# Optimization experiments

Hardware: AMD Instinct MI355X
Metric: run time of the kernel (lower is better)

## Reference

```python
import jax, jax.numpy as jnp
import numpy as np

B, S, E, H, L, NH, OUT = 32, 512, 512, 512, 2, 8, 1
HD = E // NH  # head dim


def setup_inputs() -> dict:
    key = jax.random.key(0)
    ks = jax.random.split(key, 16)
    sc_e = 1.0 / np.sqrt(E)
    sc_h = 1.0 / np.sqrt(H)
    inp = {
        "x": jax.random.normal(ks[0], (B, S, E), dtype=jnp.float32),
        "Wq": jax.random.normal(ks[1], (E, E), dtype=jnp.float32) * sc_e,
        "bq": jnp.zeros((E,), dtype=jnp.float32),
        "Wk": jax.random.normal(ks[2], (E, E), dtype=jnp.float32) * sc_e,
        "bk": jnp.zeros((E,), dtype=jnp.float32),
        "Wv": jax.random.normal(ks[3], (E, E), dtype=jnp.float32) * sc_e,
        "bv": jnp.zeros((E,), dtype=jnp.float32),
        "Wo": jax.random.normal(ks[4], (E, E), dtype=jnp.float32) * sc_e,
        "bo": jnp.zeros((E,), dtype=jnp.float32),
        # stacked RNN cell params (layer 0 input = E = H, so all layers share shape)
        "Wih": jax.random.normal(ks[5], (L, H, H), dtype=jnp.float32) * sc_h,
        "bih": jnp.zeros((L, H), dtype=jnp.float32),
        "Whh": jax.random.normal(ks[6], (L, H, H), dtype=jnp.float32) * sc_h,
        "bhh": jnp.zeros((L, H), dtype=jnp.float32),
        "Wfc": jax.random.normal(ks[7], (OUT, H), dtype=jnp.float32) * sc_h,
        "bfc": jnp.zeros((OUT,), dtype=jnp.float32),
    }
    return inp


def _forward(x, Wq, bq, Wk, bk, Wv, bv, Wo, bo, Wih, bih, Whh, bhh, Wfc, bfc):
    # Multi-head attention (self-attention, no mask; dropout = identity in eval)
    Q = (x @ Wq.T + bq).reshape(B, S, NH, HD)
    K = (x @ Wk.T + bk).reshape(B, S, NH, HD)
    V = (x @ Wv.T + bv).reshape(B, S, NH, HD)
    scores = jnp.einsum("bqhd,bkhd->bhqk", Q, K) / jnp.sqrt(jnp.float32(HD))
    attn = jax.nn.softmax(scores, axis=-1)
    ctx = jnp.einsum("bhqk,bkhd->bqhd", attn, V).reshape(B, S, E)
    atten_out = ctx @ Wo.T + bo  # [B, S, E]

    # Multi-layer Elman RNN scan over time; only last-step hidden is used.
    h0 = jnp.zeros((L, B, H), dtype=x.dtype)

    def step(h, x_t):
        inp = x_t
        new_h = []
        for i in range(L):
            inp = jnp.tanh(inp @ Wih[i].T + bih[i] + h[i] @ Whh[i].T + bhh[i])
            new_h.append(inp)
        return jnp.stack(new_h), None

    h_final, _ = jax.lax.scan(step, h0, jnp.swapaxes(atten_out, 0, 1))  # scan over S
    return h_final[-1] @ Wfc.T + bfc  # [B, OUT]


def reference(x, Wq, bq, Wk, bk, Wv, bv, Wo, bo, Wih, bih, Whh, bhh, Wfc, bfc):
    return _forward(x, Wq, bq, Wk, bk, Wv, bv, Wo, bo, Wih, bih, Whh, bhh, Wfc, bfc)
```

## Files before the change

kernel.cpp:

```cpp
#include <hip/hip_runtime.h>
#include <hip/hip_fp16.h>

#define B 32
#define S 512
#define E 512
#define H 512
#define NH 8
#define HD 64
#define POISON 0x7FC0DEADu

typedef _Float16 h16x8 __attribute__((ext_vector_type(8)));
typedef _Float16 h16x4 __attribute__((ext_vector_type(4)));
typedef _Float16 h16x2 __attribute__((ext_vector_type(2)));
typedef float f32x4 __attribute__((ext_vector_type(4)));

#if __has_builtin(__builtin_amdgcn_fdot2)
__device__ __forceinline__ float dot2f(h16x2 a, h16x2 b, float c) {
    return __builtin_amdgcn_fdot2(a, b, c, false);
}
#else
__device__ __forceinline__ float dot2f(h16x2 a, h16x2 b, float c) {
    return c + (float)a[0] * (float)b[0] + (float)a[1] * (float)b[1];
}
#endif

__device__ __forceinline__ h16x2 pr(h16x8 v, int q) {
    h16x2 r; r[0] = v[2 * q]; r[1] = v[2 * q + 1]; return r;
}

__global__ __launch_bounds__(256) void cast_h(const float* __restrict__ src,
                                              _Float16* __restrict__ dst, int n4) {
    int i = blockIdx.x * 256 + threadIdx.x;
    const int stride = gridDim.x * 256;
    for (; i < n4; i += stride) {
        float4 v = ((const float4*)src)[i];
        h16x4 o;
        o[0] = (_Float16)v.x; o[1] = (_Float16)v.y;
        o[2] = (_Float16)v.z; o[3] = (_Float16)v.w;
        ((h16x4*)dst)[i] = o;
    }
}

template <int OMODE>
__global__ __launch_bounds__(256) void gemm_mfma(const _Float16* __restrict__ A,
                                                 const _Float16* __restrict__ W,
                                                 const float* __restrict__ bias,
                                                 void* __restrict__ Cout,
                                                 int M, int N, int K) {
    __shared__ __align__(16) _Float16 Als[128 * 32];
    __shared__ __align__(16) _Float16 Bls[128 * 32];
    const int tid = threadIdx.x;
    const int m0 = blockIdx.y * 128;
    const int n0 = blockIdx.x * 128;
    const int lane = tid & 63;
    const int w = tid >> 6;
    const int wm = w >> 1, wn = w & 1;
    f32x4 acc[4][4] = {};

    const int srow = tid >> 1;
    const int shalf = tid & 1;
    const _Float16* Ag = A + (size_t)(m0 + srow) * K + shalf * 16;
    const _Float16* Wg = W + (size_t)(n0 + srow) * K + shalf * 16;

    for (int k0 = 0; k0 < K; k0 += 32) {
        h16x8 a0 = *(const h16x8*)(Ag + k0);
        h16x8 a1 = *(const h16x8*)(Ag + k0 + 8);
        h16x8 b0 = *(const h16x8*)(Wg + k0);
        h16x8 b1 = *(const h16x8*)(Wg + k0 + 8);
        __syncthreads();
        *(h16x8*)&Als[srow * 32 + shalf * 16] = a0;
        *(h16x8*)&Als[srow * 32 + shalf * 16 + 8] = a1;
        *(h16x8*)&Bls[srow * 32 + shalf * 16] = b0;
        *(h16x8*)&Bls[srow * 32 + shalf * 16 + 8] = b1;
        __syncthreads();
        h16x8 af[4], bf[4];
#pragma unroll
        for (int mt = 0; mt < 4; ++mt)
            af[mt] = *(const h16x8*)&Als[(wm * 64 + mt * 16 + (lane & 15)) * 32 + (lane >> 4) * 8];
#pragma unroll
        for (int nt = 0; nt < 4; ++nt)
            bf[nt] = *(const h16x8*)&Bls[(wn * 64 + nt * 16 + (lane & 15)) * 32 + (lane >> 4) * 8];
#pragma unroll
        for (int mt = 0; mt < 4; ++mt)
#pragma unroll
            for (int nt = 0; nt < 4; ++nt)
                acc[mt][nt] = __builtin_amdgcn_mfma_f32_16x16x32_f16(af[mt], bf[nt], acc[mt][nt], 0, 0, 0);
    }

    float* Cf = (float*)Cout;
    _Float16* Ch = (_Float16*)Cout;
    const int colb = n0 + wn * 64 + (lane & 15);
    const int rowb = m0 + wm * 64 + ((lane >> 4) << 2);
#pragma unroll
    for (int mt = 0; mt < 4; ++mt) {
#pragma unroll
        for (int nt = 0; nt < 4; ++nt) {
            const int c = colb + nt * 16;
            const float bv = bias[c];
            if (OMODE == 2) {
                const int R0 = rowb + mt * 16;
                const int bb = R0 >> 9, s = R0 & 511, hh = c >> 6, d = c & 63;
                h16x4 pk;
#pragma unroll
                for (int j = 0; j < 4; ++j) pk[j] = (_Float16)(acc[mt][nt][j] + bv);
                *(h16x4*)&Ch[((size_t)(bb * 8 + hh) * 64 + d) * 512 + s] = pk;
            } else {
#pragma unroll
                for (int j = 0; j < 4; ++j) {
                    const int R = rowb + mt * 16 + j;
                    const float v = acc[mt][nt][j] + bv;
                    if (OMODE == 0) Cf[(size_t)R * N + c] = v;
                    else if (OMODE == 3) Cf[((size_t)(R & 511) * 32 + (R >> 9)) * N + c] = v;
                    else Ch[(size_t)R * N + c] = (_Float16)v;
                }
            }
        }
    }
}

__global__ __launch_bounds__(256) void attn_mfma(_Float16* __restrict__ Qb,
                                                 const _Float16* __restrict__ Kb,
                                                 const _Float16* __restrict__ Vt) {
    __shared__ __align__(16) _Float16 Qs[64 * 72];
    __shared__ __align__(16) _Float16 Ks[64 * 72];
    __shared__ __align__(16) _Float16 Vs[64 * 72];
    __shared__ __align__(16) _Float16 Ps[4 * 16 * 72];
    const int tid = threadIdx.x;
    const int lane = tid & 63;
    const int w = tid >> 6;
    const int qt = blockIdx.x & 7;
    const int h = (blockIdx.x >> 3) & 7;
    const int b = blockIdx.x >> 6;
    const size_t qrow0 = (size_t)b * 512 + qt * 64;
    const int col0 = h * 64;

    {
        const int r = tid >> 2;
        const int c0 = (tid & 3) << 4;
        const _Float16* gq = &Qb[(qrow0 + r) * 512 + col0 + c0];
        *(h16x8*)&Qs[r * 72 + c0] = *(const h16x8*)(gq);
        *(h16x8*)&Qs[r * 72 + c0 + 8] = *(const h16x8*)(gq + 8);
    }
    __syncthreads();
    h16x8 aq[2];
#pragma unroll
    for (int ks = 0; ks < 2; ++ks)
        aq[ks] = *(const h16x8*)&Qs[(w * 16 + (lane & 15)) * 72 + ks * 32 + (lane >> 4) * 8];

    float m[4] = {-1e30f, -1e30f, -1e30f, -1e30f};
    float l[4] = {0.f, 0.f, 0.f, 0.f};
    f32x4 acco[4] = {};

    for (int kt = 0; kt < 8; ++kt) {
        __syncthreads();
        {
            const int r = tid >> 2;
            const int c0 = (tid & 3) << 4;
            const _Float16* gk = &Kb[((size_t)b * 512 + kt * 64 + r) * 512 + col0 + c0];
            *(h16x8*)&Ks[r * 72 + c0] = *(const h16x8*)(gk);
            *(h16x8*)&Ks[r * 72 + c0 + 8] = *(const h16x8*)(gk + 8);
            const _Float16* gv = &Vt[((size_t)(b * 8 + h) * 64 + r) * 512 + kt * 64 + c0];
            *(h16x8*)&Vs[r * 72 + c0] = *(const h16x8*)(gv);
            *(h16x8*)&Vs[r * 72 + c0 + 8] = *(const h16x8*)(gv + 8);
        }
        __syncthreads();
        f32x4 accs[4] = {};
#pragma unroll
        for (int nt = 0; nt < 4; ++nt) {
#pragma unroll
            for (int ks = 0; ks < 2; ++ks) {
                h16x8 bk = *(const h16x8*)&Ks[(nt * 16 + (lane & 15)) * 72 + ks * 32 + (lane >> 4) * 8];
                accs[nt] = __builtin_amdgcn_mfma_f32_16x16x32_f16(aq[ks], bk, accs[nt], 0, 0, 0);
            }
        }
#pragma unroll
        for (int j = 0; j < 4; ++j) {
            float v = fmaxf(fmaxf(accs[0][j], accs[1][j]), fmaxf(accs[2][j], accs[3][j]));
#pragma unroll
            for (int o = 1; o < 16; o <<= 1) v = fmaxf(v, __shfl_xor(v, o, 64));
            const float mn = fmaxf(m[j], v);
            const float scl = __expf(0.125f * (m[j] - mn));
            m[j] = mn;
            l[j] *= scl;
#pragma unroll
            for (int nt2 = 0; nt2 < 4; ++nt2) acco[nt2][j] *= scl;
            float ps = 0.f;
            const int prow = ((lane >> 4) << 2) + j;
#pragma unroll
            for (int nt = 0; nt < 4; ++nt) {
                const float p = __expf(0.125f * (accs[nt][j] - mn));
                ps += p;
                Ps[w * 16 * 72 + prow * 72 + nt * 16 + (lane & 15)] = (_Float16)p;
            }
#pragma unroll
            for (int o = 1; o < 16; o <<= 1) ps += __shfl_xor(ps, o, 64);
            l[j] += ps;
        }
        __syncthreads();
#pragma unroll
        for (int ks2 = 0; ks2 < 2; ++ks2) {
            h16x8 pa = *(const h16x8*)&Ps[w * 16 * 72 + (lane & 15) * 72 + ks2 * 32 + (lane >> 4) * 8];
#pragma unroll
            for (int nt2 = 0; nt2 < 4; ++nt2) {
                h16x8 bv = *(const h16x8*)&Vs[(nt2 * 16 + (lane & 15)) * 72 + ks2 * 32 + (lane >> 4) * 8];
                acco[nt2] = __builtin_amdgcn_mfma_f32_16x16x32_f16(pa, bv, acco[nt2], 0, 0, 0);
            }
        }
    }
#pragma unroll
    for (int j = 0; j < 4; ++j) {
        const float inv = 1.0f / l[j];
        const size_t r = qrow0 + w * 16 + ((lane >> 4) << 2) + j;
#pragma unroll
        for (int nt2 = 0; nt2 < 4; ++nt2)
            Qb[r * 512 + col0 + nt2 * 16 + (lane & 15)] = (_Float16)(acco[nt2][j] * inv);
    }
}

__global__ __launch_bounds__(256) void fill_poison(uint4* __restrict__ p, int n) {
    const uint4 v = {POISON, POISON, POISON, POISON};
    int i = blockIdx.x * 256 + threadIdx.x;
    const int st = gridDim.x * 256;
    for (; i < n; i += st) p[i] = v;
}

__device__ __forceinline__ unsigned long long poll2(const unsigned* p) {
    unsigned long long v = __hip_atomic_load((const unsigned long long*)p,
                                             __ATOMIC_RELAXED, __HIP_MEMORY_SCOPE_AGENT);
    while ((unsigned)v == POISON || (unsigned)(v >> 32) == POISON) {
        __builtin_amdgcn_s_sleep(1);
        v = __hip_atomic_load((const unsigned long long*)p,
                              __ATOMIC_RELAXED, __HIP_MEMORY_SCOPE_AGENT);
    }
    return v;
}

__global__ __launch_bounds__(256) void rnn_persist(const float* __restrict__ pre,
                                                   const _Float16* __restrict__ W16,
                                                   const float* __restrict__ bhh,
                                                   unsigned* __restrict__ hbuf,
                                                   _Float16* __restrict__ hbuf_h) {
    __shared__ float hl[512];
    __shared__ float part[64][17];
    const int tid = threadIdx.x;
    const int b = blockIdx.x & 31;
    const int sl = blockIdx.x >> 5;
    const int jq = tid & 15, kg = tid >> 4;
    const int jbase = sl * 64, k0 = kg * 32;
    const int j64 = tid & 63;

    const _Float16* w0p = W16 + (size_t)(jbase + jq * 4 + 0) * 512 + k0;
    const _Float16* w1p = W16 + (size_t)(jbase + jq * 4 + 1) * 512 + k0;
    const _Float16* w2p = W16 + (size_t)(jbase + jq * 4 + 2) * 512 + k0;
    const _Float16* w3p = W16 + (size_t)(jbase + jq * 4 + 3) * 512 + k0;
    const float bj = bhh[jbase + j64];

    for (int t = 0; t < S; ++t) {
        h16x8 w0[4], w1[4], w2[4], w3[4];
#pragma unroll
        for (int c8 = 0; c8 < 4; ++c8) {
            w0[c8] = *(const h16x8*)(w0p + c8 * 8);
            w1[c8] = *(const h16x8*)(w1p + c8 * 8);
            w2[c8] = *(const h16x8*)(w2p + c8 * 8);
            w3[c8] = *(const h16x8*)(w3p + c8 * 8);
        }
        const float pv = pre[((size_t)t * 32 + b) * 512 + jbase + j64];
        float a0 = 0.f, a1 = 0.f, a2 = 0.f, a3 = 0.f;
        if (t > 0) {
            const unsigned long long v = poll2(hbuf + (size_t)(t - 1) * (B * H) + b * H + tid * 2);
            hl[tid * 2] = __uint_as_float((unsigned)v);
            hl[tid * 2 + 1] = __uint_as_float((unsigned)(v >> 32));
            __syncthreads();
            f32x4 hw[8];
#pragma unroll
            for (int c = 0; c < 8; ++c) hw[c] = *(const f32x4*)&hl[k0 + c * 4];
            h16x2 hp[16];
#pragma unroll
            for (int c = 0; c < 8; ++c) {
                h16x2 p0, p1;
                p0[0] = (_Float16)hw[c][0]; p0[1] = (_Float16)hw[c][1];
                p1[0] = (_Float16)hw[c][2]; p1[1] = (_Float16)hw[c][3];
                hp[2 * c] = p0; hp[2 * c + 1] = p1;
            }
#pragma unroll
            for (int c8 = 0; c8 < 4; ++c8) {
#pragma unroll
                for (int q = 0; q < 4; ++q) {
                    a0 = dot2f(pr(w0[c8], q), hp[c8 * 4 + q], a0);
                    a1 = dot2f(pr(w1[c8], q), hp[c8 * 4 + q], a1);
                    a2 = dot2f(pr(w2[c8], q), hp[c8 * 4 + q], a2);
                    a3 = dot2f(pr(w3[c8], q), hp[c8 * 4 + q], a3);
                }
            }
        }
        part[jq * 4 + 0][kg] = a0;
        part[jq * 4 + 1][kg] = a1;
        part[jq * 4 + 2][kg] = a2;
        part[jq * 4 + 3][kg] = a3;
        __syncthreads();
        if (tid < 64) {
            float s2 = 0.f;
#pragma unroll
            for (int i = 0; i < 16; ++i) s2 += part[tid][i];
            s2 += bj + pv;
            s2 = fminf(fmaxf(s2, -15.f), 15.f);
            const float ex = __expf(2.f * s2);
            const float hval = (ex - 1.f) / (ex + 1.f);
            const size_t idx = (size_t)t * (B * H) + b * H + jbase + tid;
            __hip_atomic_store(&hbuf[idx], __float_as_uint(hval),
                               __ATOMIC_RELAXED, __HIP_MEMORY_SCOPE_AGENT);
            hbuf_h[idx] = (_Float16)hval;
        }
        __syncthreads();
    }
}

__global__ __launch_bounds__(64) void fc_out(const unsigned* __restrict__ hbits,
                                             const float* __restrict__ Wfc,
                                             const float* __restrict__ bfc,
                                             float* __restrict__ out) {
    int b = blockIdx.x;
    int t = threadIdx.x;
    float a = 0.f;
    for (int j = t; j < 512; j += 64) a += __uint_as_float(hbits[b * 512 + j]) * Wfc[j];
#pragma unroll
    for (int o = 32; o; o >>= 1) a += __shfl_down(a, o, 64);
    if (t == 0) out[b] = a + bfc[0];
}

extern "C" void kernel_launch(void* const* d_in, const int* in_sizes, int n_in,
                              void* d_out, int out_size, void* d_ws, size_t ws_size,
                              hipStream_t stream) {
    const float* x   = (const float*)d_in[0];
    const float* Wq  = (const float*)d_in[1];
    const float* bq  = (const float*)d_in[2];
    const float* Wk  = (const float*)d_in[3];
    const float* bk  = (const float*)d_in[4];
    const float* Wv  = (const float*)d_in[5];
    const float* bv  = (const float*)d_in[6];
    const float* Wo  = (const float*)d_in[7];
    const float* bo  = (const float*)d_in[8];
    const float* Wih = (const float*)d_in[9];
    const float* bih = (const float*)d_in[10];
    const float* Whh = (const float*)d_in[11];
    const float* bhh = (const float*)d_in[12];
    const float* Wfc = (const float*)d_in[13];
    const float* bfc = (const float*)d_in[14];
    float* out = (float*)d_out;
    char* base = (char*)d_ws;

    _Float16* xh   = (_Float16*)(base);
    unsigned* h0u  = (unsigned*)(base);
    _Float16* Qh   = (_Float16*)(base + ((size_t)32 << 20));
    _Float16* h0h  = (_Float16*)(base + ((size_t)32 << 20));
    _Float16* Kh   = (_Float16*)(base + ((size_t)48 << 20));
    unsigned* h1u  = (unsigned*)(base + ((size_t)48 << 20));
    _Float16* Vth  = (_Float16*)(base + ((size_t)64 << 20));
    float*    pre  = (float*)(base + ((size_t)80 << 20));
    _Float16* wgt  = (_Float16*)(base + ((size_t)112 << 20));
    const size_t WSZ = 512 * 512;

    cast_h<<<dim3(4096), dim3(256), 0, stream>>>(x, xh, (B * S * E) / 4);
    cast_h<<<dim3(256), dim3(256), 0, stream>>>(Wq, wgt + 0 * WSZ, WSZ / 4);
    cast_h<<<dim3(256), dim3(256), 0, stream>>>(Wk, wgt + 1 * WSZ, WSZ / 4);
    cast_h<<<dim3(256), dim3(256), 0, stream>>>(Wv, wgt + 2 * WSZ, WSZ / 4);
    cast_h<<<dim3(256), dim3(256), 0, stream>>>(Wo, wgt + 3 * WSZ, WSZ / 4);
    cast_h<<<dim3(256), dim3(256), 0, stream>>>(Wih, wgt + 4 * WSZ, WSZ / 4);
    cast_h<<<dim3(256), dim3(256), 0, stream>>>(Wih + WSZ, wgt + 5 * WSZ, WSZ / 4);
    cast_h<<<dim3(256), dim3(256), 0, stream>>>(Whh, wgt + 6 * WSZ, WSZ / 4);
    cast_h<<<dim3(256), dim3(256), 0, stream>>>(Whh + WSZ, wgt + 7 * WSZ, WSZ / 4);

    const dim3 gg(4, 128), blk(256);
    gemm_mfma<1><<<gg, blk, 0, stream>>>(xh, wgt + 0 * WSZ, bq, Qh, B * S, E, E);
    gemm_mfma<1><<<gg, blk, 0, stream>>>(xh, wgt + 1 * WSZ, bk, Kh, B * S, E, E);
    gemm_mfma<2><<<gg, blk, 0, stream>>>(xh, wgt + 2 * WSZ, bv, Vth, B * S, E, E);
    attn_mfma<<<dim3(B * NH * 8), blk, 0, stream>>>(Qh, Kh, Vth);
    gemm_mfma<1><<<gg, blk, 0, stream>>>(Qh, wgt + 3 * WSZ, bo, Kh, B * S, E, E);
    gemm_mfma<3><<<gg, blk, 0, stream>>>(Kh, wgt + 4 * WSZ, bih, pre, B * S, H, E);

    fill_poison<<<dim3(1024), blk, 0, stream>>>((uint4*)base, (32 << 20) / 16);
    rnn_persist<<<dim3(256), blk, 0, stream>>>(pre, wgt + 6 * WSZ, bhh, h0u, h0h);
    gemm_mfma<0><<<gg, blk, 0, stream>>>(h0h, wgt + 5 * WSZ, bih + 512, pre, B * S, H, H);
    fill_poison<<<dim3(1024), blk, 0, stream>>>((uint4*)(base + ((size_t)48 << 20)),
                                                (32 << 20) / 16);
    rnn_persist<<<dim3(256), blk, 0, stream>>>(pre, wgt + 7 * WSZ, bhh + 512, h1u, h0h);
    fc_out<<<dim3(32), dim3(64), 0, stream>>>(h1u + (size_t)511 * B * H, Wfc, bfc, out);
}
```

Measured before the change: 1.223 ms.

## Fuse both RNN layers into one persistent kernel with LDS-resident recurrent weights

Replaces the two sequential per-layer persistent RNN launches and the intermediate input-projection GEMM with a single 512-block kernel. Half the blocks run layer 0 and half run layer 1, and layer 1 consumes layer 0's hidden states through poll-on-poison as they are produced. Each layer's Whh slice is staged once into swizzled LDS (64KB) instead of being reloaded from global memory every step. Layer 1 now computes its Wih projection inline each step, reading those weights from global memory. The scheme relies on all 512 blocks being co-resident (2 per CU) to avoid deadlock.

```diff
diff --git a/kernel.cpp b/kernel.cpp
--- a/kernel.cpp
+++ b/kernel.cpp
@@ -109,8 +109,7 @@
                 for (int j = 0; j < 4; ++j) {
                     const int R = rowb + mt * 16 + j;
                     const float v = acc[mt][nt][j] + bv;
-                    if (OMODE == 0) Cf[(size_t)R * N + c] = v;
-                    else if (OMODE == 3) Cf[((size_t)(R & 511) * 32 + (R >> 9)) * N + c] = v;
+                    if (OMODE == 3) Cf[((size_t)(R & 511) * 32 + (R >> 9)) * N + c] = v;
                     else Ch[(size_t)R * N + c] = (_Float16)v;
                 }
             }
@@ -235,45 +234,62 @@
     return v;
 }
 
-__global__ __launch_bounds__(256) void rnn_persist(const float* __restrict__ pre,
-                                                   const _Float16* __restrict__ W16,
-                                                   const float* __restrict__ bhh,
-                                                   unsigned* __restrict__ hbuf,
-                                                   _Float16* __restrict__ hbuf_h) {
-    __shared__ float hl[512];
+__global__ __launch_bounds__(256, 2) void rnn_fused2(const float* __restrict__ pre0,
+                                                     const _Float16* __restrict__ Whh0h,
+                                                     const _Float16* __restrict__ Whh1h,
+                                                     const _Float16* __restrict__ Wih1h,
+                                                     const float* __restrict__ bhh,
+                                                     const float* __restrict__ bih,
+                                                     unsigned* __restrict__ h0u,
+                                                     unsigned* __restrict__ h1u) {
+    __shared__ __align__(16) _Float16 Wl[64 * 512];
+    __shared__ float hlA[512];
+    __shared__ float hlB[512];
     __shared__ float part[64][17];
     const int tid = threadIdx.x;
+    const int role = blockIdx.x >> 8;
     const int b = blockIdx.x & 31;
-    const int sl = blockIdx.x >> 5;
+    const int sl = (blockIdx.x >> 5) & 7;
     const int jq = tid & 15, kg = tid >> 4;
     const int jbase = sl * 64, k0 = kg * 32;
     const int j64 = tid & 63;
 
-    const _Float16* w0p = W16 + (size_t)(jbase + jq * 4 + 0) * 512 + k0;
-    const _Float16* w1p = W16 + (size_t)(jbase + jq * 4 + 1) * 512 + k0;
-    const _Float16* w2p = W16 + (size_t)(jbase + jq * 4 + 2) * 512 + k0;
-    const _Float16* w3p = W16 + (size_t)(jbase + jq * 4 + 3) * 512 + k0;
-    const float bj = bhh[jbase + j64];
+    const _Float16* Wsrc = role ? Whh1h : Whh0h;
+#pragma unroll
+    for (int i = 0; i < 16; ++i) {
+        const int e = tid + i * 256;
+        const int row = e >> 6;
+        const int l = e & 63;
+        h16x8 v = *(const h16x8*)&Wsrc[(size_t)(jbase + row) * 512 + l * 8];
+        const int p = (l & 56) | ((l + (row >> 2)) & 7);
+        *(h16x8*)&Wl[row * 512 + p * 8] = v;
+    }
+    const float bconst = role ? (bih[512 + jbase + j64] + bhh[512 + jbase + j64])
+                              : bhh[jbase + j64];
+    unsigned* myH = role ? h1u : h0u;
+    __syncthreads();
 
     for (int t = 0; t < S; ++t) {
-        h16x8 w0[4], w1[4], w2[4], w3[4];
-#pragma unroll
-        for (int c8 = 0; c8 < 4; ++c8) {
-            w0[c8] = *(const h16x8*)(w0p + c8 * 8);
-            w1[c8] = *(const h16x8*)(w1p + c8 * 8);
-            w2[c8] = *(const h16x8*)(w2p + c8 * 8);
-            w3[c8] = *(const h16x8*)(w3p + c8 * 8);
-        }
-        const float pv = pre[((size_t)t * 32 + b) * 512 + jbase + j64];
         float a0 = 0.f, a1 = 0.f, a2 = 0.f, a3 = 0.f;
-        if (t > 0) {
-            const unsigned long long v = poll2(hbuf + (size_t)(t - 1) * (B * H) + b * H + tid * 2);
-            hl[tid * 2] = __uint_as_float((unsigned)v);
-            hl[tid * 2 + 1] = __uint_as_float((unsigned)(v >> 32));
+        float pv = 0.f;
+        if (role == 0) {
+            pv = pre0[((size_t)t * 32 + b) * 512 + jbase + j64];
+        } else {
+            h16x8 ww0[4], ww1[4], ww2[4], ww3[4];
+#pragma unroll
+            for (int c8 = 0; c8 < 4; ++c8) {
+                ww0[c8] = *(const h16x8*)&Wih1h[(size_t)(jbase + jq * 4 + 0) * 512 + k0 + c8 * 8];
+                ww1[c8] = *(const h16x8*)&Wih1h[(size_t)(jbase + jq * 4 + 1) * 512 + k0 + c8 * 8];
+                ww2[c8] = *(const h16x8*)&Wih1h[(size_t)(jbase + jq * 4 + 2) * 512 + k0 + c8 * 8];
+                ww3[c8] = *(const h16x8*)&Wih1h[(size_t)(jbase + jq * 4 + 3) * 512 + k0 + c8 * 8];
+            }
+            const unsigned long long v = poll2(h0u + (size_t)t * (B * H) + b * H + tid * 2);
+            hlA[tid * 2] = __uint_as_float((unsigned)v);
+            hlA[tid * 2 + 1] = __uint_as_float((unsigned)(v >> 32));
             __syncthreads();
             f32x4 hw[8];
 #pragma unroll
-            for (int c = 0; c < 8; ++c) hw[c] = *(const f32x4*)&hl[k0 + c * 4];
+            for (int c = 0; c < 8; ++c) hw[c] = *(const f32x4*)&hlA[k0 + c * 4];
             h16x2 hp[16];
 #pragma unroll
             for (int c = 0; c < 8; ++c) {
@@ -286,11 +302,43 @@
             for (int c8 = 0; c8 < 4; ++c8) {
 #pragma unroll
                 for (int q = 0; q < 4; ++q) {
-                    a0 = dot2f(pr(w0[c8], q), hp[c8 * 4 + q], a0);
-                    a1 = dot2f(pr(w1[c8], q), hp[c8 * 4 + q], a1);
-                    a2 = dot2f(pr(w2[c8], q), hp[c8 * 4 + q], a2);
-                    a3 = dot2f(pr(w3[c8], q), hp[c8 * 4 + q], a3);
+                    a0 = dot2f(pr(ww0[c8], q), hp[c8 * 4 + q], a0);
+                    a1 = dot2f(pr(ww1[c8], q), hp[c8 * 4 + q], a1);
+                    a2 = dot2f(pr(ww2[c8], q), hp[c8 * 4 + q], a2);
+                    a3 = dot2f(pr(ww3[c8], q), hp[c8 * 4 + q], a3);
                 }
+            }
+        }
+        if (t > 0) {
+            const unsigned long long v = poll2(myH + (size_t)(t - 1) * (B * H) + b * H + tid * 2);
+            hlB[tid * 2] = __uint_as_float((unsigned)v);
+            hlB[tid * 2 + 1] = __uint_as_float((unsigned)(v >> 32));
+            __syncthreads();
+            f32x4 hw[8];
+#pragma unroll
+            for (int c = 0; c < 8; ++c) hw[c] = *(const f32x4*)&hlB[k0 + c * 4];
+            h16x2 hp[16];
+#pragma unroll
+            for (int c = 0; c < 8; ++c) {
+                h16x2 p0, p1;
+                p0[0] = (_Float16)hw[c][0]; p0[1] = (_Float16)hw[c][1];
+                p1[0] = (_Float16)hw[c][2]; p1[1] = (_Float16)hw[c][3];
+                hp[2 * c] = p0; hp[2 * c + 1] = p1;
+            }
+#pragma unroll
+            for (int jj = 0; jj < 4; ++jj) {
+                const int r = jq * 4 + jj;
+                float s = 0.f;
+#pragma unroll
+                for (int c8 = 0; c8 < 4; ++c8) {
+                    const int l = kg * 4 + c8;
+                    const int p = (l & 56) | ((l + jq) & 7);
+                    h16x8 w8 = *(const h16x8*)&Wl[r * 512 + p * 8];
+#pragma unroll
+                    for (int q = 0; q < 4; ++q) s = dot2f(pr(w8, q), hp[c8 * 4 + q], s);
+                }
+                if (jj == 0) a0 += s; else if (jj == 1) a1 += s;
+                else if (jj == 2) a2 += s; else a3 += s;
             }
         }
         part[jq * 4 + 0][kg] = a0;
@@ -302,14 +350,13 @@
             float s2 = 0.f;
 #pragma unroll
             for (int i = 0; i < 16; ++i) s2 += part[tid][i];
-            s2 += bj + pv;
+            s2 += bconst + pv;
             s2 = fminf(fmaxf(s2, -15.f), 15.f);
             const float ex = __expf(2.f * s2);
             const float hval = (ex - 1.f) / (ex + 1.f);
-            const size_t idx = (size_t)t * (B * H) + b * H + jbase + tid;
-            __hip_atomic_store(&hbuf[idx], __float_as_uint(hval),
-                               __ATOMIC_RELAXED, __HIP_MEMORY_SCOPE_AGENT);
-            hbuf_h[idx] = (_Float16)hval;
+            __hip_atomic_store(&myH[(size_t)t * (B * H) + b * H + jbase + tid],
+                               __float_as_uint(hval), __ATOMIC_RELAXED,
+                               __HIP_MEMORY_SCOPE_AGENT);
         }
         __syncthreads();
     }
@@ -352,7 +399,6 @@
     _Float16* xh   = (_Float16*)(base);
     unsigned* h0u  = (unsigned*)(base);
     _Float16* Qh   = (_Float16*)(base + ((size_t)32 << 20));
-    _Float16* h0h  = (_Float16*)(base + ((size_t)32 << 20));
     _Float16* Kh   = (_Float16*)(base + ((size_t)48 << 20));
     unsigned* h1u  = (unsigned*)(base + ((size_t)48 << 20));
     _Float16* Vth  = (_Float16*)(base + ((size_t)64 << 20));
@@ -379,10 +425,9 @@
     gemm_mfma<3><<<gg, blk, 0, stream>>>(Kh, wgt + 4 * WSZ, bih, pre, B * S, H, E);
 
     fill_poison<<<dim3(1024), blk, 0, stream>>>((uint4*)base, (32 << 20) / 16);
-    rnn_persist<<<dim3(256), blk, 0, stream>>>(pre, wgt + 6 * WSZ, bhh, h0u, h0h);
-    gemm_mfma<0><<<gg, blk, 0, stream>>>(h0h, wgt + 5 * WSZ, bih + 512, pre, B * S, H, H);
     fill_poison<<<dim3(1024), blk, 0, stream>>>((uint4*)(base + ((size_t)48 << 20)),
                                                 (32 << 20) / 16);
-    rnn_persist<<<dim3(256), blk, 0, stream>>>(pre, wgt + 7 * WSZ, bhh + 512, h1u, h0h);
+    rnn_fused2<<<dim3(512), blk, 0, stream>>>(pre, wgt + 6 * WSZ, wgt + 7 * WSZ,
+                                              wgt + 5 * WSZ, bhh, bih, h0u, h1u);
     fc_out<<<dim3(32), dim3(64), 0, stream>>>(h1u + (size_t)511 * B * H, Wfc, bfc, out);
 }
```

After: 1.912 ms. 1.56x slower.

## Restructure persistent RNN step: LDS-resident weights, fp16 packed state, shuffle reduction

Applied to the files above, without the earlier changes.

The persistent RNN kernel now stages its 64x512 fp16 weight slice in shared memory once, instead of reloading it from global memory every timestep. The hidden state is exchanged between blocks as packed fp16 pairs, so one buffer serves both polling and the next GEMM. Each thread polls its own slice of the state directly, with no LDS staging or barrier. The cross-thread reduction uses 16-lane xor shuffles instead of an LDS partial-sum array and two __syncthreads. This cuts per-step barriers and memory traffic on the latency-bound recurrence, in exchange for fp16 rounding of the exchanged state and a larger shared-memory footprint (64 KB per block).

```diff
diff --git a/kernel.cpp b/kernel.cpp
--- a/kernel.cpp
+++ b/kernel.cpp
@@ -26,6 +26,14 @@
 
 __device__ __forceinline__ h16x2 pr(h16x8 v, int q) {
     h16x2 r; r[0] = v[2 * q]; r[1] = v[2 * q + 1]; return r;
+}
+__device__ __forceinline__ h16x2 asp(unsigned u) {
+    return __builtin_bit_cast(h16x2, u);
+}
+__device__ __forceinline__ unsigned pack2(float x, float y) {
+    unsigned short a = __builtin_bit_cast(unsigned short, (_Float16)x);
+    unsigned short b = __builtin_bit_cast(unsigned short, (_Float16)y);
+    return ((unsigned)b << 16) | (unsigned)a;
 }
 
 __global__ __launch_bounds__(256) void cast_h(const float* __restrict__ src,
@@ -224,105 +232,112 @@
     for (; i < n; i += st) p[i] = v;
 }
 
-__device__ __forceinline__ unsigned long long poll2(const unsigned* p) {
-    unsigned long long v = __hip_atomic_load((const unsigned long long*)p,
-                                             __ATOMIC_RELAXED, __HIP_MEMORY_SCOPE_AGENT);
-    while ((unsigned)v == POISON || (unsigned)(v >> 32) == POISON) {
-        __builtin_amdgcn_s_sleep(1);
-        v = __hip_atomic_load((const unsigned long long*)p,
-                              __ATOMIC_RELAXED, __HIP_MEMORY_SCOPE_AGENT);
-    }
-    return v;
-}
-
 __global__ __launch_bounds__(256) void rnn_persist(const float* __restrict__ pre,
                                                    const _Float16* __restrict__ W16,
                                                    const float* __restrict__ bhh,
-                                                   unsigned* __restrict__ hbuf,
-                                                   _Float16* __restrict__ hbuf_h) {
-    __shared__ float hl[512];
-    __shared__ float part[64][17];
+                                                   unsigned* __restrict__ hu) {
+    __shared__ __align__(16) _Float16 Wl[64 * 512];
     const int tid = threadIdx.x;
     const int b = blockIdx.x & 31;
     const int sl = blockIdx.x >> 5;
-    const int jq = tid & 15, kg = tid >> 4;
-    const int jbase = sl * 64, k0 = kg * 32;
-    const int j64 = tid & 63;
-
-    const _Float16* w0p = W16 + (size_t)(jbase + jq * 4 + 0) * 512 + k0;
-    const _Float16* w1p = W16 + (size_t)(jbase + jq * 4 + 1) * 512 + k0;
-    const _Float16* w2p = W16 + (size_t)(jbase + jq * 4 + 2) * 512 + k0;
-    const _Float16* w3p = W16 + (size_t)(jbase + jq * 4 + 3) * 512 + k0;
-    const float bj = bhh[jbase + j64];
+    const int jq = tid >> 4;
+    const int kg = tid & 15;
+    const int jbase = sl * 64;
+
+#pragma unroll
+    for (int i = 0; i < 16; ++i) {
+        const int e = tid + i * 256;
+        const int row = e >> 6;
+        const int l = e & 63;
+        *(h16x8*)&Wl[row * 512 + l * 8] =
+            *(const h16x8*)&W16[(size_t)(jbase + row) * 512 + l * 8];
+    }
+    const int jp = jq * 4 + (kg & 1) * 2;
+    const float bj0 = bhh[jbase + jp];
+    const float bj1 = bhh[jbase + jp + 1];
+    __syncthreads();
 
     for (int t = 0; t < S; ++t) {
         h16x8 w0[4], w1[4], w2[4], w3[4];
 #pragma unroll
         for (int c8 = 0; c8 < 4; ++c8) {
-            w0[c8] = *(const h16x8*)(w0p + c8 * 8);
-            w1[c8] = *(const h16x8*)(w1p + c8 * 8);
-            w2[c8] = *(const h16x8*)(w2p + c8 * 8);
-            w3[c8] = *(const h16x8*)(w3p + c8 * 8);
-        }
-        const float pv = pre[((size_t)t * 32 + b) * 512 + jbase + j64];
+            const int l8 = (16 * c8 + kg) * 8;
+            w0[c8] = *(const h16x8*)&Wl[(jq * 4 + 0) * 512 + l8];
+            w1[c8] = *(const h16x8*)&Wl[(jq * 4 + 1) * 512 + l8];
+            w2[c8] = *(const h16x8*)&Wl[(jq * 4 + 2) * 512 + l8];
+            w3[c8] = *(const h16x8*)&Wl[(jq * 4 + 3) * 512 + l8];
+        }
+        const float2 pv = *(const float2*)&pre[((size_t)t * 32 + b) * 512 + jbase + jp];
         float a0 = 0.f, a1 = 0.f, a2 = 0.f, a3 = 0.f;
         if (t > 0) {
-            const unsigned long long v = poll2(hbuf + (size_t)(t - 1) * (B * H) + b * H + tid * 2);
-            hl[tid * 2] = __uint_as_float((unsigned)v);
-            hl[tid * 2 + 1] = __uint_as_float((unsigned)(v >> 32));
-            __syncthreads();
-            f32x4 hw[8];
-#pragma unroll
-            for (int c = 0; c < 8; ++c) hw[c] = *(const f32x4*)&hl[k0 + c * 4];
-            h16x2 hp[16];
-#pragma unroll
-            for (int c = 0; c < 8; ++c) {
-                h16x2 p0, p1;
-                p0[0] = (_Float16)hw[c][0]; p0[1] = (_Float16)hw[c][1];
-                p1[0] = (_Float16)hw[c][2]; p1[1] = (_Float16)hw[c][3];
-                hp[2 * c] = p0; hp[2 * c + 1] = p1;
+            const unsigned long long* src =
+                (const unsigned long long*)(hu + (size_t)(t - 1) * (B * H / 2) + b * 256);
+            unsigned long long v[8];
+            bool again = true;
+            while (again) {
+#pragma unroll
+                for (int c8 = 0; c8 < 4; ++c8) {
+                    const int u2 = (16 * c8 + kg) * 2;
+                    v[c8 * 2 + 0] = __hip_atomic_load(src + u2, __ATOMIC_RELAXED,
+                                                      __HIP_MEMORY_SCOPE_AGENT);
+                    v[c8 * 2 + 1] = __hip_atomic_load(src + u2 + 1, __ATOMIC_RELAXED,
+                                                      __HIP_MEMORY_SCOPE_AGENT);
+                }
+                again = false;
+#pragma unroll
+                for (int i = 0; i < 8; ++i) {
+                    if ((unsigned)v[i] == POISON || (unsigned)(v[i] >> 32) == POISON)
+                        again = true;
+                }
+                if (again) __builtin_amdgcn_s_sleep(1);
             }
 #pragma unroll
             for (int c8 = 0; c8 < 4; ++c8) {
+                h16x2 hpx[4];
+                hpx[0] = asp((unsigned)v[c8 * 2 + 0]);
+                hpx[1] = asp((unsigned)(v[c8 * 2 + 0] >> 32));
+                hpx[2] = asp((unsigned)v[c8 * 2 + 1]);
+                hpx[3] = asp((unsigned)(v[c8 * 2 + 1] >> 32));
 #pragma unroll
                 for (int q = 0; q < 4; ++q) {
-                    a0 = dot2f(pr(w0[c8], q), hp[c8 * 4 + q], a0);
-                    a1 = dot2f(pr(w1[c8], q), hp[c8 * 4 + q], a1);
-                    a2 = dot2f(pr(w2[c8], q), hp[c8 * 4 + q], a2);
-                    a3 = dot2f(pr(w3[c8], q), hp[c8 * 4 + q], a3);
+                    a0 = dot2f(pr(w0[c8], q), hpx[q], a0);
+                    a1 = dot2f(pr(w1[c8], q), hpx[q], a1);
+                    a2 = dot2f(pr(w2[c8], q), hpx[q], a2);
+                    a3 = dot2f(pr(w3[c8], q), hpx[q], a3);
                 }
             }
         }
-        part[jq * 4 + 0][kg] = a0;
-        part[jq * 4 + 1][kg] = a1;
-        part[jq * 4 + 2][kg] = a2;
-        part[jq * 4 + 3][kg] = a3;
-        __syncthreads();
-        if (tid < 64) {
-            float s2 = 0.f;
-#pragma unroll
-            for (int i = 0; i < 16; ++i) s2 += part[tid][i];
-            s2 += bj + pv;
-            s2 = fminf(fmaxf(s2, -15.f), 15.f);
-            const float ex = __expf(2.f * s2);
-            const float hval = (ex - 1.f) / (ex + 1.f);
-            const size_t idx = (size_t)t * (B * H) + b * H + jbase + tid;
-            __hip_atomic_store(&hbuf[idx], __float_as_uint(hval),
-                               __ATOMIC_RELAXED, __HIP_MEMORY_SCOPE_AGENT);
-            hbuf_h[idx] = (_Float16)hval;
-        }
-        __syncthreads();
-    }
-}
-
-__global__ __launch_bounds__(64) void fc_out(const unsigned* __restrict__ hbits,
+#pragma unroll
+        for (int o = 1; o < 16; o <<= 1) {
+            a0 += __shfl_xor(a0, o, 16);
+            a1 += __shfl_xor(a1, o, 16);
+            a2 += __shfl_xor(a2, o, 16);
+            a3 += __shfl_xor(a3, o, 16);
+        }
+        if (kg < 2) {
+            const float sa = (kg == 0) ? a0 : a2;
+            const float sb = (kg == 0) ? a1 : a3;
+            float s0 = sa + pv.x + bj0;
+            float s1 = sb + pv.y + bj1;
+            s0 = fminf(fmaxf(s0, -15.f), 15.f);
+            s1 = fminf(fmaxf(s1, -15.f), 15.f);
+            const float e0 = __expf(2.f * s0), e1 = __expf(2.f * s1);
+            const float h0 = (e0 - 1.f) / (e0 + 1.f);
+            const float h1 = (e1 - 1.f) / (e1 + 1.f);
+            __hip_atomic_store(&hu[(size_t)t * (B * H / 2) + b * 256 + (jbase + jp) / 2],
+                               pack2(h0, h1), __ATOMIC_RELAXED, __HIP_MEMORY_SCOPE_AGENT);
+        }
+    }
+}
+
+__global__ __launch_bounds__(64) void fc_out(const _Float16* __restrict__ hh,
                                              const float* __restrict__ Wfc,
                                              const float* __restrict__ bfc,
                                              float* __restrict__ out) {
     int b = blockIdx.x;
     int t = threadIdx.x;
     float a = 0.f;
-    for (int j = t; j < 512; j += 64) a += __uint_as_float(hbits[b * 512 + j]) * Wfc[j];
+    for (int j = t; j < 512; j += 64) a += (float)hh[b * 512 + j] * Wfc[j];
 #pragma unroll
     for (int o = 32; o; o >>= 1) a += __shfl_down(a, o, 64);
     if (t == 0) out[b] = a + bfc[0];
@@ -351,10 +366,11 @@
 
     _Float16* xh   = (_Float16*)(base);
     unsigned* h0u  = (unsigned*)(base);
+    _Float16* h0h  = (_Float16*)(base);
     _Float16* Qh   = (_Float16*)(base + ((size_t)32 << 20));
-    _Float16* h0h  = (_Float16*)(base + ((size_t)32 << 20));
     _Float16* Kh   = (_Float16*)(base + ((size_t)48 << 20));
     unsigned* h1u  = (unsigned*)(base + ((size_t)48 << 20));
+    _Float16* h1h  = (_Float16*)(base + ((size_t)48 << 20));
     _Float16* Vth  = (_Float16*)(base + ((size_t)64 << 20));
     float*    pre  = (float*)(base + ((size_t)80 << 20));
     _Float16* wgt  = (_Float16*)(base + ((size_t)112 << 20));
@@ -378,11 +394,11 @@
     gemm_mfma<1><<<gg, blk, 0, stream>>>(Qh, wgt + 3 * WSZ, bo, Kh, B * S, E, E);
     gemm_mfma<3><<<gg, blk, 0, stream>>>(Kh, wgt + 4 * WSZ, bih, pre, B * S, H, E);
 
-    fill_poison<<<dim3(1024), blk, 0, stream>>>((uint4*)base, (32 << 20) / 16);
-    rnn_persist<<<dim3(256), blk, 0, stream>>>(pre, wgt + 6 * WSZ, bhh, h0u, h0h);
+    fill_poison<<<dim3(1024), blk, 0, stream>>>((uint4*)base, (16 << 20) / 16);
+    rnn_persist<<<dim3(256), blk, 0, stream>>>(pre, wgt + 6 * WSZ, bhh, h0u);
     gemm_mfma<0><<<gg, blk, 0, stream>>>(h0h, wgt + 5 * WSZ, bih + 512, pre, B * S, H, H);
     fill_poison<<<dim3(1024), blk, 0, stream>>>((uint4*)(base + ((size_t)48 << 20)),
-                                                (32 << 20) / 16);
-    rnn_persist<<<dim3(256), blk, 0, stream>>>(pre, wgt + 7 * WSZ, bhh + 512, h1u, h0h);
-    fc_out<<<dim3(32), dim3(64), 0, stream>>>(h1u + (size_t)511 * B * H, Wfc, bfc, out);
-}
+                                                (16 << 20) / 16);
+    rnn_persist<<<dim3(256), blk, 0, stream>>>(pre, wgt + 7 * WSZ, bhh + 512, h1u);
+    fc_out<<<dim3(32), dim3(64), 0, stream>>>(h1h + (size_t)511 * B * H, Wfc, bfc, out);
+}
```

Measured after the change: 2.744 ms. +124.3%, slower.
